# Kernel optimization log

Hardware: AMD Instinct MI355X
Metric: run time of the kernel (lower is better)

The kernel has to match this reference:

```python
import jax, jax.numpy as jnp
import numpy as np

B, N = 2, 8192
D_POINTS, D_MODEL, K = 64, 128, 16


def _lin(key, fi, fo):
    return jax.random.normal(key, (fi, fo), jnp.float32) / np.sqrt(fi)


def setup_inputs() -> dict:
    key = jax.random.key(0)
    ks = jax.random.split(key, 16)
    return {
        "xyz": jax.random.normal(ks[0], (B, N, 3), jnp.float32),
        "normals": jax.random.normal(ks[1], (B, N, 3), jnp.float32),
        "features": jax.random.normal(ks[2], (B, N, D_POINTS), jnp.float32),
        "fc1_w": _lin(ks[3], D_POINTS, D_MODEL), "fc1_b": jnp.zeros((D_MODEL,), jnp.float32),
        "fc2_w": _lin(ks[4], D_MODEL, D_POINTS), "fc2_b": jnp.zeros((D_POINTS,), jnp.float32),
        "gamma_w1": _lin(ks[5], D_MODEL, D_MODEL), "gamma_b1": jnp.zeros((D_MODEL,), jnp.float32),
        "gamma_w2": _lin(ks[6], D_MODEL, D_MODEL), "gamma_b2": jnp.zeros((D_MODEL,), jnp.float32),
        "delta_w1": _lin(ks[7], 3, D_MODEL), "delta_b1": jnp.zeros((D_MODEL,), jnp.float32),
        "delta_w2": _lin(ks[8], D_MODEL, D_MODEL), "delta_b2": jnp.zeros((D_MODEL,), jnp.float32),
        "wq": _lin(ks[9], D_MODEL, D_MODEL),
        "wk": _lin(ks[10], D_MODEL, D_MODEL),
        "wv": _lin(ks[11], D_MODEL, D_MODEL),
    }


def _gather(points, idx):
    # points: (b, n, c), idx: (b, n, k) -> (b, n, k, c)
    b, n, c = points.shape
    k = idx.shape[-1]
    flat = jnp.take_along_axis(points, idx.reshape(b, n * k, 1), axis=1)
    return flat.reshape(b, n, k, c)


def reference(xyz, normals, features, fc1_w, fc1_b, fc2_w, fc2_b,
              gamma_w1, gamma_b1, gamma_w2, gamma_b2,
              delta_w1, delta_b1, delta_w2, delta_b2, wq, wk, wv):
    # pairwise squared distances (b, n, n)
    sq = jnp.sum(xyz * xyz, axis=-1)
    dists = sq[:, :, None] + sq[:, None, :] - 2.0 * jnp.einsum('bnd,bmd->bnm', xyz, xyz)
    _, knn_idx = jax.lax.top_k(-dists, K)  # k smallest distances (includes self)

    knn_xyz = _gather(xyz, knn_idx)                      # (b, n, k, 3)
    x = features @ fc1_w + fc1_b                         # (b, n, d_model)
    q = x @ wq                                           # (b, n, d_model)
    k_nbr = _gather(x @ wk, knn_idx)                     # (b, n, k, d_model)
    v_nbr = _gather(x @ wv, knn_idx)                     # (b, n, k, d_model)

    # positional encoding: fc_delta(rel_pos), ends with ReLU
    rel = xyz[:, :, None, :] - knn_xyz                   # (b, n, k, 3)
    pos_enc = jax.nn.relu(jax.nn.relu(rel @ delta_w1 + delta_b1) @ delta_w2 + delta_b2)

    # vector attention logits: fc_gamma(q - k + pos_enc)
    h = q[:, :, None, :] - k_nbr + pos_enc
    logits = jax.nn.relu(h @ gamma_w1 + gamma_b1) @ gamma_w2 + gamma_b2
    attn = jax.nn.softmax(logits / np.sqrt(D_MODEL), axis=-2)  # softmax over neighbors

    res = jnp.einsum('bnkf,bnkf->bnf', attn, v_nbr + pos_enc)
    res = res @ fc2_w + fc2_b + features
    return res, attn
```

## Files before the change

### kernel.cpp

```cpp
#include <hip/hip_runtime.h>
#include <cstdint>

typedef unsigned long long ull;
typedef __bf16 bf16x8 __attribute__((ext_vector_type(8)));
typedef float f32x4 __attribute__((ext_vector_type(4)));
typedef float f32x2 __attribute__((ext_vector_type(2)));

#define NPTS 8192
#define NB 2
#define KNN 16
#define DM 128
#define PADK 136

__device__ __forceinline__ float sq3f(float x, float y, float z) {
    return __fadd_rn(__fadd_rn(__fmul_rn(x, x), __fmul_rn(y, y)), __fmul_rn(z, z));
}
__device__ __forceinline__ unsigned ford(unsigned u) {
    return (u & 0x80000000u) ? ~u : (u | 0x80000000u);
}
__device__ __forceinline__ float inv_ford(unsigned f) {
    unsigned u = (f & 0x80000000u) ? (f ^ 0x80000000u) : ~f;
    return __uint_as_float(u);
}
__device__ __forceinline__ f32x2 pk_mul(f32x2 a, f32x2 b) {
    f32x2 d;
    asm("v_pk_mul_f32 %0, %1, %2" : "=v"(d) : "v"(a), "v"(b));
    return d;
}
__device__ __forceinline__ f32x2 pk_add(f32x2 a, f32x2 b) {
    f32x2 d;
    asm("v_pk_add_f32 %0, %1, %2" : "=v"(d) : "v"(a), "v"(b));
    return d;
}

__global__ __launch_bounds__(256) void knn_kernel(const float* __restrict__ xyz,
                                                  int* __restrict__ idx_out) {
    __shared__ float4 xsA[512];
    __shared__ float4 xsB[512];
    const int t = threadIdx.x;
    const int wv = t >> 6, lane = t & 63;
    const int q_id = blockIdx.x * 4 + wv;
    const int b = q_id >> 13;
    const int i = q_id & (NPTS - 1);
    const float* xb = xyz + (size_t)b * NPTS * 3;
    const float qx = xb[3 * i + 0], qy = xb[3 * i + 1], qz = xb[3 * i + 2];
    const float sqi = sq3f(qx, qy, qz);
    const f32x2 qx2 = {qx, qx}, qy2 = {qy, qy}, qz2 = {qz, qz};
    const f32x2 sqi2 = {sqi, sqi}, ntwo2 = {-2.0f, -2.0f};

    unsigned list_hi = 0xffffffffu, list_lo = 0xffffffffu;
    float thrF = __uint_as_float(0x7f800000u);

#define INSERT(FC, CKLO)                                                                 \
    {                                                                                    \
        unsigned ck_hi = ford(__float_as_uint(FC));                                      \
        unsigned ck_lo = (CKLO);                                                         \
        unsigned ph = __shfl_up(list_hi, 1);                                             \
        unsigned pl = __shfl_up(list_lo, 1);                                             \
        bool lt = (ck_hi < list_hi) || (ck_hi == list_hi && ck_lo < list_lo);            \
        bool ge = (lane == 0) || (ck_hi > ph) || (ck_hi == ph && ck_lo >= pl);           \
        list_hi = lt ? (ge ? ck_hi : ph) : list_hi;                                      \
        list_lo = lt ? (ge ? ck_lo : pl) : list_lo;                                      \
        unsigned th = (unsigned)__builtin_amdgcn_readlane((int)list_hi, 15);             \
        th = (th > 0xff800000u) ? 0xff800000u : th;            \
        thrF = fminf(thrF, inv_ford(th));                                                \
    }

    for (int ch = 0; ch < 8; ++ch) {
        __syncthreads();
#pragma unroll
        for (int e = 0; e < 2; e++) {
            int s = t + e * 256;
            int c0 = ((s >> 6) << 7) + (s & 63);
            int g = ch * 1024 + c0;
            float x0 = xb[3 * g + 0], y0 = xb[3 * g + 1], z0 = xb[3 * g + 2];
            float x1 = xb[3 * (g + 64) + 0], y1 = xb[3 * (g + 64) + 1], z1 = xb[3 * (g + 64) + 2];
            xsA[s] = make_float4(x0, x1, y0, y1);
            xsB[s] = make_float4(z0, z1, sq3f(x0, y0, z0), sq3f(x1, y1, z1));
        }
        __syncthreads();
        for (int m = 0; m < 8; m++) {
            const int s = m * 64 + lane;
            float4 A = xsA[s];
            float4 B = xsB[s];
            f32x2 ax = {A.x, A.y}, ay = {A.z, A.w};
            f32x2 bz = {B.x, B.y}, bs = {B.z, B.w};
            f32x2 p1 = pk_mul(qx2, ax);
            f32x2 p2 = pk_mul(qy2, ay);
            f32x2 p3 = pk_mul(qz2, bz);
            f32x2 s1 = pk_add(p1, p2);
            f32x2 s2 = pk_add(s1, p3);
            f32x2 num = pk_add(sqi2, bs);
            f32x2 tm = pk_mul(ntwo2, s2);
            f32x2 dd = pk_add(num, tm);
            float dA = dd.x, dB = dd.y;
            if (ch == 0 && m == 0) {
                float mn = fminf(dA, dB);
                mn = fminf(mn, __shfl_xor(mn, 1));
                mn = fminf(mn, __shfl_xor(mn, 2));
                float mx = mn;
                mx = fmaxf(mx, __shfl_xor(mx, 4));
                mx = fmaxf(mx, __shfl_xor(mx, 8));
                mx = fmaxf(mx, __shfl_xor(mx, 16));
                mx = fmaxf(mx, __shfl_xor(mx, 32));
                thrF = mx;
            }
            ull balA = __ballot(dA <= thrF);
            ull balB = __ballot(dB <= thrF);
            if ((balA | balB) == 0ull) continue;
            const unsigned jbase = (unsigned)(ch * 1024 + m * 128);
            while (balA) {
                int l = (int)__builtin_ctzll(balA);
                balA &= balA - 1;
                float fc = __uint_as_float(
                    (unsigned)__builtin_amdgcn_readlane(__float_as_int(dA), l));
                if (fc <= thrF) INSERT(fc, jbase + (unsigned)l)
            }
            while (balB) {
                int l = (int)__builtin_ctzll(balB);
                balB &= balB - 1;
                float fc = __uint_as_float(
                    (unsigned)__builtin_amdgcn_readlane(__float_as_int(dB), l));
                if (fc <= thrF) INSERT(fc, jbase + 64u + (unsigned)l)
            }
        }
    }
#undef INSERT
    if (lane < 16)
        idx_out[q_id * 16 + lane] = (int)list_lo;
}

__global__ __launch_bounds__(256) void wprep_kernel(const float* __restrict__ d2,
                                                    const float* __restrict__ g1,
                                                    const float* __restrict__ g2,
                                                    const float* __restrict__ wq,
                                                    const float* __restrict__ wk,
                                                    const float* __restrict__ wv,
                                                    __bf16* __restrict__ d2t,
                                                    __bf16* __restrict__ g1t,
                                                    __bf16* __restrict__ g2t,
                                                    __bf16* __restrict__ wqt,
                                                    __bf16* __restrict__ wkt,
                                                    __bf16* __restrict__ wvt) {
    const int bi = blockIdx.x;
    const float* src = (bi == 0) ? d2 : (bi == 1) ? g1 : (bi == 2) ? g2
                     : (bi == 3) ? wq : (bi == 4) ? wk : wv;
    __bf16* dst = (bi == 0) ? d2t : (bi == 1) ? g1t : (bi == 2) ? g2t
                : (bi == 3) ? wqt : (bi == 4) ? wkt : wvt;
#pragma unroll
    for (int e = 0; e < 64; e++) {
        int id = threadIdx.x + e * 256;
        int k = id >> 7, n = id & 127;
        dst[n * 128 + k] = (__bf16)src[id];
    }
}

#define STAGE_W(SRC)                                                                       \
    {                                                                                      \
        _Pragma("unroll")                                                                  \
        for (int e = 0; e < 8; e++) {                                                      \
            int ch = t + e * 256;                                                          \
            int r = ch >> 4, ck = ch & 15;                                                 \
            *(bf16x8*)&Wb[r * PADK + ck * 8] = *(const bf16x8*)&SRC[r * 128 + ck * 8];     \
        }                                                                                  \
    }

__global__ __launch_bounds__(256, 1) void xqkv_kernel(const float* __restrict__ feats,
                                                      const float* __restrict__ fc1_w,
                                                      const float* __restrict__ fc1_b,
                                                      const __bf16* __restrict__ wqt,
                                                      const __bf16* __restrict__ wkt,
                                                      const __bf16* __restrict__ wvt,
                                                      float* __restrict__ qo,
                                                      float* __restrict__ ko,
                                                      float* __restrict__ vo) {
    __shared__ __align__(16) char lds[52224];
    float* At = (float*)lds;
    float* Wt = (float*)(lds + 16640);
    __bf16* Ab = (__bf16*)lds;
    __bf16* Wb = (__bf16*)(lds + 17408);
    const int t = threadIdx.x;
    const int base = blockIdx.x * 64;

#pragma unroll
    for (int e = 0; e < 16; e++) {
        int id = t + e * 256;
        int r = id >> 6, c = id & 63;
        At[c * 65 + r] = feats[(size_t)(base + r) * 64 + c];
    }
#pragma unroll
    for (int e = 0; e < 32; e++) { int id = t + e * 256; Wt[id] = fc1_w[id]; }
    __syncthreads();
    const int r0 = (t >> 4) * 4;
    const int c0 = (t & 15) * 8;
    float acc[4][8];
#pragma unroll
    for (int i = 0; i < 4; i++)
#pragma unroll
        for (int j = 0; j < 8; j++) acc[i][j] = fc1_b[c0 + j];
#pragma unroll 4
    for (int kk = 0; kk < 64; ++kk) {
        float a0 = At[kk * 65 + r0 + 0];
        float a1 = At[kk * 65 + r0 + 1];
        float a2 = At[kk * 65 + r0 + 2];
        float a3 = At[kk * 65 + r0 + 3];
        const float4 w0 = *(const float4*)&Wt[kk * 128 + c0];
        const float4 w1 = *(const float4*)&Wt[kk * 128 + c0 + 4];
        float wj[8] = {w0.x, w0.y, w0.z, w0.w, w1.x, w1.y, w1.z, w1.w};
#pragma unroll
        for (int j = 0; j < 8; j++) {
            acc[0][j] += a0 * wj[j];
            acc[1][j] += a1 * wj[j];
            acc[2][j] += a2 * wj[j];
            acc[3][j] += a3 * wj[j];
        }
    }
    __syncthreads();

#pragma unroll
    for (int i = 0; i < 4; i++)
#pragma unroll
        for (int j = 0; j < 8; j++)
            Ab[(r0 + i) * PADK + c0 + j] = (__bf16)acc[i][j];
    STAGE_W(wqt)
    __syncthreads();

    const int lane = t & 63;
    const int lr = lane & 15, lg = lane >> 4;
    const int rbase = (t >> 6) * 16;

#define QGEMM(ACC, OUT)                                                                    \
    {                                                                                      \
        f32x4 ACC[8];                                                                      \
        _Pragma("unroll")                                                                  \
        for (int ct = 0; ct < 8; ct++) ACC[ct] = (f32x4){0.f, 0.f, 0.f, 0.f};              \
        _Pragma("unroll")                                                                  \
        for (int kt = 0; kt < 4; kt++) {                                                   \
            const int ko = kt * 32 + 8 * lg;                                               \
            bf16x8 a0 = *(const bf16x8*)&Ab[(rbase + lr) * PADK + ko];                     \
            _Pragma("unroll")                                                              \
            for (int ct = 0; ct < 8; ct++) {                                               \
                bf16x8 bv = *(const bf16x8*)&Wb[(ct * 16 + lr) * PADK + ko];               \
                ACC[ct] = __builtin_amdgcn_mfma_f32_16x16x32_bf16(a0, bv, ACC[ct], 0, 0, 0); \
            }                                                                              \
        }                                                                                  \
        _Pragma("unroll")                                                                  \
        for (int ct = 0; ct < 8; ct++)                                                     \
            _Pragma("unroll")                                                              \
            for (int e = 0; e < 4; e++)                                                    \
                OUT[(size_t)(base + rbase + 4 * lg + e) * 128 + ct * 16 + lr] = ACC[ct][e]; \
    }

    QGEMM(accq, qo)
    __syncthreads();
    STAGE_W(wkt)
    __syncthreads();
    QGEMM(acck, ko)
    __syncthreads();
    STAGE_W(wvt)
    __syncthreads();
    QGEMM(accv, vo)
#undef QGEMM
}

#define DO_GEMM(ACC0, ACC1, WPTR)                                                          \
    {                                                                                      \
        _Pragma("unroll")                                                                  \
        for (int kt = 0; kt < 4; kt++) {                                                   \
            const int ko = kt * 32 + 8 * lg;                                               \
            bf16x8 a0 = *(const bf16x8*)&Ab[(rbase + lr) * PADK + ko];                     \
            bf16x8 a1 = *(const bf16x8*)&Ab[(rbase + 16 + lr) * PADK + ko];                \
            _Pragma("unroll")                                                              \
            for (int ct = 0; ct < 8; ct++) {                                               \
                bf16x8 bv = *(const bf16x8*)&WPTR[(ct * 16 + lr) * PADK + ko];             \
                ACC0[ct] = __builtin_amdgcn_mfma_f32_16x16x32_bf16(a0, bv, ACC0[ct], 0, 0, 0); \
                ACC1[ct] = __builtin_amdgcn_mfma_f32_16x16x32_bf16(a1, bv, ACC1[ct], 0, 0, 0); \
            }                                                                              \
        }                                                                                  \
    }

__global__ __launch_bounds__(256, 2) void k345_kernel(const float* __restrict__ xyz,
                                                      const int* __restrict__ idxw,
                                                      const float* __restrict__ q,
                                                      const float* __restrict__ xk,
                                                      const float* __restrict__ xv,
                                                      const float* __restrict__ d1,
                                                      const float* __restrict__ bd1,
                                                      const float* __restrict__ bd2,
                                                      const float* __restrict__ bg1,
                                                      const float* __restrict__ bg2,
                                                      const __bf16* __restrict__ d2t,
                                                      const __bf16* __restrict__ g1t,
                                                      const __bf16* __restrict__ g2t,
                                                      float* __restrict__ attn,
                                                      float* __restrict__ res_pre) {
    __shared__ __bf16 Ab[128 * PADK];
    __shared__ __bf16 Wb[128 * PADK];
    __shared__ float rels[128 * 4];
    __shared__ int jrow[128];
    __shared__ float d1s[3 * 128];
    __shared__ float bd1s[128], bd2s[128], bg1s[128], bg2s[128];

    const int t = threadIdx.x;
    const int wv = t >> 6;
    const int lane = t & 63;
    const int lr = lane & 15, lg = lane >> 4;
    const int R0 = blockIdx.x * 128;
    const int b = R0 >> 17;
    const int rbase = wv * 32;

#pragma unroll
    for (int e = 0; e < 2; e++) { int id = t + e * 256; if (id < 384) d1s[id] = d1[id]; }
    if (t < 128) {
        bd1s[t] = bd1[t]; bd2s[t] = bd2[t]; bg1s[t] = bg1[t]; bg2s[t] = bg2[t];
    } else {
        int r = t - 128;
        int j = idxw[R0 + r];
        jrow[r] = j;
        const float* pn = xyz + (size_t)((R0 + r) >> 4) * 3;
        const float* pj = xyz + (size_t)((b << 13) + j) * 3;
        rels[r * 4 + 0] = pn[0] - pj[0];
        rels[r * 4 + 1] = pn[1] - pj[1];
        rels[r * 4 + 2] = pn[2] - pj[2];
    }
    STAGE_W(d2t)
    __syncthreads();

    {
        const int c = t & 127;
        const float w0 = d1s[c], w1 = d1s[128 + c], w2 = d1s[256 + c], bb = bd1s[c];
#pragma unroll
        for (int e = 0; e < 64; e++) {
            int r = (t >> 7) + e * 2;
            float v = fmaf(rels[r * 4 + 2], w2,
                      fmaf(rels[r * 4 + 1], w1, fmaf(rels[r * 4 + 0], w0, bb)));
            Ab[r * PADK + c] = (__bf16)fmaxf(v, 0.0f);
        }
    }
    __syncthreads();

    f32x4 acc0[8], acc1[8];
#pragma unroll
    for (int ct = 0; ct < 8; ct++) {
        float bb = bd2s[ct * 16 + lr];
        acc0[ct] = (f32x4){bb, bb, bb, bb};
        acc1[ct] = acc0[ct];
    }
    DO_GEMM(acc0, acc1, Wb)
    f32x4 pos0[8], pos1[8];
#pragma unroll
    for (int ct = 0; ct < 8; ct++) {
#pragma unroll
        for (int e = 0; e < 4; e++) {
            pos0[ct][e] = fmaxf(acc0[ct][e], 0.0f);
            pos1[ct][e] = fmaxf(acc1[ct][e], 0.0f);
        }
    }

#pragma unroll
    for (int rt = 0; rt < 2; rt++) {
        const int rloc = rbase + rt * 16 + 4 * lg;
        const size_t qbase = (size_t)((R0 + rloc) >> 4) * 128;
        const int j0 = jrow[rloc + 0], j1 = jrow[rloc + 1];
        const int j2 = jrow[rloc + 2], j3 = jrow[rloc + 3];
        const size_t kb0 = (size_t)((b << 13) + j0) * 128;
        const size_t kb1 = (size_t)((b << 13) + j1) * 128;
        const size_t kb2 = (size_t)((b << 13) + j2) * 128;
        const size_t kb3 = (size_t)((b << 13) + j3) * 128;
        f32x4* posR = rt ? pos1 : pos0;
#pragma unroll
        for (int ct = 0; ct < 8; ct++) {
            const int c = ct * 16 + lr;
            const float qv = q[qbase + c];
            f32x4 p = posR[ct];
            Ab[(rloc + 0) * PADK + c] = (__bf16)(p[0] + qv - xk[kb0 + c]);
            Ab[(rloc + 1) * PADK + c] = (__bf16)(p[1] + qv - xk[kb1 + c]);
            Ab[(rloc + 2) * PADK + c] = (__bf16)(p[2] + qv - xk[kb2 + c]);
            Ab[(rloc + 3) * PADK + c] = (__bf16)(p[3] + qv - xk[kb3 + c]);
        }
    }
    __syncthreads();
    STAGE_W(g1t)
    __syncthreads();

#pragma unroll
    for (int ct = 0; ct < 8; ct++) {
        float bb = bg1s[ct * 16 + lr];
        acc0[ct] = (f32x4){bb, bb, bb, bb};
        acc1[ct] = acc0[ct];
    }
    DO_GEMM(acc0, acc1, Wb)
#pragma unroll
    for (int rt = 0; rt < 2; rt++) {
        const int rloc = rbase + rt * 16 + 4 * lg;
        f32x4* accR = rt ? acc1 : acc0;
#pragma unroll
        for (int ct = 0; ct < 8; ct++) {
            const int c = ct * 16 + lr;
            f32x4 p = accR[ct];
            Ab[(rloc + 0) * PADK + c] = (__bf16)fmaxf(p[0], 0.0f);
            Ab[(rloc + 1) * PADK + c] = (__bf16)fmaxf(p[1], 0.0f);
            Ab[(rloc + 2) * PADK + c] = (__bf16)fmaxf(p[2], 0.0f);
            Ab[(rloc + 3) * PADK + c] = (__bf16)fmaxf(p[3], 0.0f);
        }
    }
    __syncthreads();
    STAGE_W(g2t)
    __syncthreads();

#pragma unroll
    for (int ct = 0; ct < 8; ct++) {
        float bb = bg2s[ct * 16 + lr];
        acc0[ct] = (f32x4){bb, bb, bb, bb};
        acc1[ct] = acc0[ct];
    }
    DO_GEMM(acc0, acc1, Wb)
    const float scale = 0.08838834764831845f;
#pragma unroll
    for (int rt = 0; rt < 2; rt++) {
        const int rloc = rbase + rt * 16 + 4 * lg;
        const int j0 = jrow[rloc + 0], j1 = jrow[rloc + 1];
        const int j2 = jrow[rloc + 2], j3 = jrow[rloc + 3];
        const size_t vb0 = (size_t)((b << 13) + j0) * 128;
        const size_t vb1 = (size_t)((b << 13) + j1) * 128;
        const size_t vb2 = (size_t)((b << 13) + j2) * 128;
        const size_t vb3 = (size_t)((b << 13) + j3) * 128;
        f32x4* accR = rt ? acc1 : acc0;
        f32x4* posR = rt ? pos1 : pos0;
#pragma unroll
        for (int ct = 0; ct < 8; ct++) {
            const int c = ct * 16 + lr;
            f32x4 p = accR[ct];
            float l0 = p[0] * scale, l1 = p[1] * scale, l2 = p[2] * scale, l3 = p[3] * scale;
            float m = fmaxf(fmaxf(l0, l1), fmaxf(l2, l3));
            m = fmaxf(m, __shfl_xor(m, 16));
            m = fmaxf(m, __shfl_xor(m, 32));
            float e0 = __expf(l0 - m), e1 = __expf(l1 - m);
            float e2 = __expf(l2 - m), e3 = __expf(l3 - m);
            float s = (e0 + e1) + (e2 + e3);
            s += __shfl_xor(s, 16);
            s += __shfl_xor(s, 32);
            float inv = 1.0f / s;
            float a0 = e0 * inv, a1 = e1 * inv, a2 = e2 * inv, a3 = e3 * inv;
            size_t ob = (size_t)(R0 + rloc) * 128 + c;
            attn[ob + 0 * 128] = a0;
            attn[ob + 1 * 128] = a1;
            attn[ob + 2 * 128] = a2;
            attn[ob + 3 * 128] = a3;
            f32x4 pp = posR[ct];
            float r = a0 * (xv[vb0 + c] + pp[0])
                    + a1 * (xv[vb1 + c] + pp[1])
                    + a2 * (xv[vb2 + c] + pp[2])
                    + a3 * (xv[vb3 + c] + pp[3]);
            r += __shfl_xor(r, 16);
            r += __shfl_xor(r, 32);
            if (lg == 0)
                res_pre[(size_t)((R0 >> 4) + wv * 2 + rt) * 128 + c] = r;
        }
    }
}

__global__ __launch_bounds__(256, 1) void k6_kernel(const float* __restrict__ res_pre,
                                                    const float* __restrict__ w,
                                                    const float* __restrict__ bias,
                                                    const float* __restrict__ feats,
                                                    float* __restrict__ res_out) {
    __shared__ float At[128 * 65];
    __shared__ __align__(16) float Wt[128 * 64];
    const int t = threadIdx.x;
    const int base = blockIdx.x * 64;
#pragma unroll
    for (int e = 0; e < 32; e++) {
        int id = t + e * 256;
        int r = id >> 7, c = id & 127;
        At[c * 65 + r] = res_pre[(size_t)(base + r) * 128 + c];
    }
#pragma unroll
    for (int e = 0; e < 32; e++) { int id = t + e * 256; Wt[id] = w[id]; }
    __syncthreads();
    const int r0 = (t >> 4) * 4;
    const int c0 = (t & 15) * 4;
    float acc[4][4];
#pragma unroll
    for (int i = 0; i < 4; i++)
#pragma unroll
        for (int j = 0; j < 4; j++) acc[i][j] = bias[c0 + j];
#pragma unroll 4
    for (int kk = 0; kk < 128; ++kk) {
        float a0 = At[kk * 65 + r0 + 0];
        float a1 = At[kk * 65 + r0 + 1];
        float a2 = At[kk * 65 + r0 + 2];
        float a3 = At[kk * 65 + r0 + 3];
        const float4 w0 = *(const float4*)&Wt[kk * 64 + c0];
        float wj[4] = {w0.x, w0.y, w0.z, w0.w};
#pragma unroll
        for (int j = 0; j < 4; j++) {
            acc[0][j] += a0 * wj[j];
            acc[1][j] += a1 * wj[j];
            acc[2][j] += a2 * wj[j];
            acc[3][j] += a3 * wj[j];
        }
    }
#pragma unroll
    for (int i = 0; i < 4; i++)
#pragma unroll
        for (int j = 0; j < 4; j++)
            res_out[(size_t)(base + r0 + i) * 64 + c0 + j] =
                acc[i][j] + feats[(size_t)(base + r0 + i) * 64 + c0 + j];
}

extern "C" void kernel_launch(void* const* d_in, const int* in_sizes, int n_in,
                              void* d_out, int out_size, void* d_ws, size_t ws_size,
                              hipStream_t stream) {
    (void)in_sizes; (void)n_in; (void)out_size; (void)ws_size;
    const float* xyz   = (const float*)d_in[0];
    const float* feats = (const float*)d_in[2];
    const float* fc1_w = (const float*)d_in[3];
    const float* fc1_b = (const float*)d_in[4];
    const float* fc2_w = (const float*)d_in[5];
    const float* fc2_b = (const float*)d_in[6];
    const float* g1    = (const float*)d_in[7];
    const float* bg1   = (const float*)d_in[8];
    const float* g2    = (const float*)d_in[9];
    const float* bg2   = (const float*)d_in[10];
    const float* d1    = (const float*)d_in[11];
    const float* bd1   = (const float*)d_in[12];
    const float* d2    = (const float*)d_in[13];
    const float* bd2   = (const float*)d_in[14];
    const float* wq    = (const float*)d_in[15];
    const float* wk    = (const float*)d_in[16];
    const float* wv    = (const float*)d_in[17];

    int* idxw   = (int*)d_ws;
    float* qbuf = (float*)((char*)d_ws + (1 << 20));
    float* kbuf = qbuf + 2097152;
    float* vbuf = kbuf + 2097152;
    float* rpre = vbuf + 2097152;
    __bf16* d2t = (__bf16*)(rpre + 2097152);
    __bf16* g1t = d2t + 16384;
    __bf16* g2t = g1t + 16384;
    __bf16* wqt = g2t + 16384;
    __bf16* wkt = wqt + 16384;
    __bf16* wvt = wkt + 16384;

    float* res_out = (float*)d_out;
    float* attn    = res_out + 1048576;

    wprep_kernel<<<6, 256, 0, stream>>>(d2, g1, g2, wq, wk, wv,
                                        d2t, g1t, g2t, wqt, wkt, wvt);
    knn_kernel<<<4096, 256, 0, stream>>>(xyz, idxw);
    xqkv_kernel<<<256, 256, 0, stream>>>(feats, fc1_w, fc1_b, wqt, wkt, wvt,
                                         qbuf, kbuf, vbuf);
    k345_kernel<<<2048, 256, 0, stream>>>(xyz, idxw, qbuf, kbuf, vbuf, d1, bd1, bd2, bg1, bg2,
                                          d2t, g1t, g2t, attn, rpre);
    k6_kernel<<<256, 256, 0, stream>>>(rpre, fc2_w, fc2_b, feats, res_out);
}
```

Baseline: 244.5 us.

## Merge KNN and QKV projection into one launch with block-index dispatch

Combines the KNN search kernel and the x/q/k/v projection kernel into a single launch. The first 256 blocks run the projection and the rest run the KNN, so the small GEMM work overlaps the KNN instead of running after it. The projection no longer stages weights in LDS and reads fc1_w and the bf16 q/k/v weights straight from global memory. This shrinks shared memory to 17 KB and allows higher occupancy (launch bound 6). The trade-off is uncoalesced or repeated global weight reads, plus possible register pressure from the shared launch bound.

```diff
diff --git a/kernel.cpp b/kernel.cpp
--- a/kernel.cpp
+++ b/kernel.cpp
@@ -33,13 +33,14 @@
     return d;
 }
 
-__global__ __launch_bounds__(256) void knn_kernel(const float* __restrict__ xyz,
-                                                  int* __restrict__ idx_out) {
-    __shared__ float4 xsA[512];
-    __shared__ float4 xsB[512];
+__device__ __forceinline__ void knn_body(const float* __restrict__ xyz,
+                                         int* __restrict__ idx_out,
+                                         char* lds, int bid) {
+    float4* xsA = (float4*)lds;
+    float4* xsB = (float4*)(lds + 8192);
     const int t = threadIdx.x;
     const int wv = t >> 6, lane = t & 63;
-    const int q_id = blockIdx.x * 4 + wv;
+    const int q_id = bid * 4 + wv;
     const int b = q_id >> 13;
     const int i = q_id & (NPTS - 1);
     const float* xb = xyz + (size_t)b * NPTS * 3;
@@ -130,6 +131,111 @@
         idx_out[q_id * 16 + lane] = (int)list_lo;
 }
 
+__device__ __forceinline__ void xqkv_body(const float* __restrict__ feats,
+                                          const float* __restrict__ fc1_w,
+                                          const float* __restrict__ fc1_b,
+                                          const __bf16* __restrict__ wqt,
+                                          const __bf16* __restrict__ wkt,
+                                          const __bf16* __restrict__ wvt,
+                                          float* __restrict__ qo,
+                                          float* __restrict__ kko,
+                                          float* __restrict__ vvo,
+                                          char* lds, int bid) {
+    float* At = (float*)lds;
+    __bf16* Ab = (__bf16*)lds;
+    const int t = threadIdx.x;
+    const int base = bid * 64;
+
+#pragma unroll
+    for (int e = 0; e < 16; e++) {
+        int id = t + e * 256;
+        int r = id >> 6, c = id & 63;
+        At[c * 65 + r] = feats[(size_t)(base + r) * 64 + c];
+    }
+    __syncthreads();
+    const int r0 = (t >> 4) * 4;
+    const int c0 = (t & 15) * 8;
+    float acc[4][8];
+#pragma unroll
+    for (int i = 0; i < 4; i++)
+#pragma unroll
+        for (int j = 0; j < 8; j++) acc[i][j] = fc1_b[c0 + j];
+#pragma unroll 4
+    for (int kk = 0; kk < 64; ++kk) {
+        float a0 = At[kk * 65 + r0 + 0];
+        float a1 = At[kk * 65 + r0 + 1];
+        float a2 = At[kk * 65 + r0 + 2];
+        float a3 = At[kk * 65 + r0 + 3];
+        const float4 w0 = *(const float4*)&fc1_w[kk * 128 + c0];
+        const float4 w1 = *(const float4*)&fc1_w[kk * 128 + c0 + 4];
+        float wj[8] = {w0.x, w0.y, w0.z, w0.w, w1.x, w1.y, w1.z, w1.w};
+#pragma unroll
+        for (int j = 0; j < 8; j++) {
+            acc[0][j] += a0 * wj[j];
+            acc[1][j] += a1 * wj[j];
+            acc[2][j] += a2 * wj[j];
+            acc[3][j] += a3 * wj[j];
+        }
+    }
+    __syncthreads();
+
+#pragma unroll
+    for (int i = 0; i < 4; i++)
+#pragma unroll
+        for (int j = 0; j < 8; j++)
+            Ab[(r0 + i) * PADK + c0 + j] = (__bf16)acc[i][j];
+    __syncthreads();
+
+    const int lane = t & 63;
+    const int lr = lane & 15, lg = lane >> 4;
+    const int rbase = (t >> 6) * 16;
+
+#define QGEMM(WPTR, OUT)                                                                   \
+    {                                                                                      \
+        f32x4 accg[8];                                                                     \
+        _Pragma("unroll")                                                                  \
+        for (int ct = 0; ct < 8; ct++) accg[ct] = (f32x4){0.f, 0.f, 0.f, 0.f};             \
+        _Pragma("unroll")                                                                  \
+        for (int kt = 0; kt < 4; kt++) {                                                   \
+            const int ko = kt * 32 + 8 * lg;                                               \
+            bf16x8 a0 = *(const bf16x8*)&Ab[(rbase + lr) * PADK + ko];                     \
+            _Pragma("unroll")                                                              \
+            for (int ct = 0; ct < 8; ct++) {                                               \
+                bf16x8 bv = *(const bf16x8*)&WPTR[(ct * 16 + lr) * 128 + ko];              \
+                accg[ct] = __builtin_amdgcn_mfma_f32_16x16x32_bf16(a0, bv, accg[ct], 0, 0, 0); \
+            }                                                                              \
+        }                                                                                  \
+        _Pragma("unroll")                                                                  \
+        for (int ct = 0; ct < 8; ct++)                                                     \
+            _Pragma("unroll")                                                              \
+            for (int e = 0; e < 4; e++)                                                    \
+                OUT[(size_t)(base + rbase + 4 * lg + e) * 128 + ct * 16 + lr] = accg[ct][e]; \
+    }
+
+    QGEMM(wqt, qo)
+    QGEMM(wkt, kko)
+    QGEMM(wvt, vvo)
+#undef QGEMM
+}
+
+__global__ __launch_bounds__(256, 6) void mega_kernel(const float* __restrict__ xyz,
+                                                      int* __restrict__ idxw,
+                                                      const float* __restrict__ feats,
+                                                      const float* __restrict__ fc1_w,
+                                                      const float* __restrict__ fc1_b,
+                                                      const __bf16* __restrict__ wqt,
+                                                      const __bf16* __restrict__ wkt,
+                                                      const __bf16* __restrict__ wvt,
+                                                      float* __restrict__ qo,
+                                                      float* __restrict__ kko,
+                                                      float* __restrict__ vvo) {
+    __shared__ __align__(16) char lds[17408];
+    if (blockIdx.x < 256)
+        xqkv_body(feats, fc1_w, fc1_b, wqt, wkt, wvt, qo, kko, vvo, lds, blockIdx.x);
+    else
+        knn_body(xyz, idxw, lds, blockIdx.x - 256);
+}
+
 __global__ __launch_bounds__(256) void wprep_kernel(const float* __restrict__ d2,
                                                     const float* __restrict__ g1,
                                                     const float* __restrict__ g2,
@@ -164,104 +270,6 @@
             *(bf16x8*)&Wb[r * PADK + ck * 8] = *(const bf16x8*)&SRC[r * 128 + ck * 8];     \
         }                                                                                  \
     }
-
-__global__ __launch_bounds__(256, 1) void xqkv_kernel(const float* __restrict__ feats,
-                                                      const float* __restrict__ fc1_w,
-                                                      const float* __restrict__ fc1_b,
-                                                      const __bf16* __restrict__ wqt,
-                                                      const __bf16* __restrict__ wkt,
-                                                      const __bf16* __restrict__ wvt,
-                                                      float* __restrict__ qo,
-                                                      float* __restrict__ ko,
-                                                      float* __restrict__ vo) {
-    __shared__ __align__(16) char lds[52224];
-    float* At = (float*)lds;
-    float* Wt = (float*)(lds + 16640);
-    __bf16* Ab = (__bf16*)lds;
-    __bf16* Wb = (__bf16*)(lds + 17408);
-    const int t = threadIdx.x;
-    const int base = blockIdx.x * 64;
-
-#pragma unroll
-    for (int e = 0; e < 16; e++) {
-        int id = t + e * 256;
-        int r = id >> 6, c = id & 63;
-        At[c * 65 + r] = feats[(size_t)(base + r) * 64 + c];
-    }
-#pragma unroll
-    for (int e = 0; e < 32; e++) { int id = t + e * 256; Wt[id] = fc1_w[id]; }
-    __syncthreads();
-    const int r0 = (t >> 4) * 4;
-    const int c0 = (t & 15) * 8;
-    float acc[4][8];
-#pragma unroll
-    for (int i = 0; i < 4; i++)
-#pragma unroll
-        for (int j = 0; j < 8; j++) acc[i][j] = fc1_b[c0 + j];
-#pragma unroll 4
-    for (int kk = 0; kk < 64; ++kk) {
-        float a0 = At[kk * 65 + r0 + 0];
-        float a1 = At[kk * 65 + r0 + 1];
-        float a2 = At[kk * 65 + r0 + 2];
-        float a3 = At[kk * 65 + r0 + 3];
-        const float4 w0 = *(const float4*)&Wt[kk * 128 + c0];
-        const float4 w1 = *(const float4*)&Wt[kk * 128 + c0 + 4];
-        float wj[8] = {w0.x, w0.y, w0.z, w0.w, w1.x, w1.y, w1.z, w1.w};
-#pragma unroll
-        for (int j = 0; j < 8; j++) {
-            acc[0][j] += a0 * wj[j];
-            acc[1][j] += a1 * wj[j];
-            acc[2][j] += a2 * wj[j];
-            acc[3][j] += a3 * wj[j];
-        }
-    }
-    __syncthreads();
-
-#pragma unroll
-    for (int i = 0; i < 4; i++)
-#pragma unroll
-        for (int j = 0; j < 8; j++)
-            Ab[(r0 + i) * PADK + c0 + j] = (__bf16)acc[i][j];
-    STAGE_W(wqt)
-    __syncthreads();
-
-    const int lane = t & 63;
-    const int lr = lane & 15, lg = lane >> 4;
-    const int rbase = (t >> 6) * 16;
-
-#define QGEMM(ACC, OUT)                                                                    \
-    {                                                                                      \
-        f32x4 ACC[8];                                                                      \
-        _Pragma("unroll")                                                                  \
-        for (int ct = 0; ct < 8; ct++) ACC[ct] = (f32x4){0.f, 0.f, 0.f, 0.f};              \
-        _Pragma("unroll")                                                                  \
-        for (int kt = 0; kt < 4; kt++) {                                                   \
-            const int ko = kt * 32 + 8 * lg;                                               \
-            bf16x8 a0 = *(const bf16x8*)&Ab[(rbase + lr) * PADK + ko];                     \
-            _Pragma("unroll")                                                              \
-            for (int ct = 0; ct < 8; ct++) {                                               \
-                bf16x8 bv = *(const bf16x8*)&Wb[(ct * 16 + lr) * PADK + ko];               \
-                ACC[ct] = __builtin_amdgcn_mfma_f32_16x16x32_bf16(a0, bv, ACC[ct], 0, 0, 0); \
-            }                                                                              \
-        }                                                                                  \
-        _Pragma("unroll")                                                                  \
-        for (int ct = 0; ct < 8; ct++)                                                     \
-            _Pragma("unroll")                                                              \
-            for (int e = 0; e < 4; e++)                                                    \
-                OUT[(size_t)(base + rbase + 4 * lg + e) * 128 + ct * 16 + lr] = ACC[ct][e]; \
-    }
-
-    QGEMM(accq, qo)
-    __syncthreads();
-    STAGE_W(wkt)
-    __syncthreads();
-    QGEMM(acck, ko)
-    __syncthreads();
-    STAGE_W(wvt)
-    __syncthreads();
-    QGEMM(accv, vo)
-#undef QGEMM
-}
 
 #define DO_GEMM(ACC0, ACC1, WPTR)                                                          \
     {                                                                                      \
@@ -548,9 +556,8 @@
 
     wprep_kernel<<<6, 256, 0, stream>>>(d2, g1, g2, wq, wk, wv,
                                         d2t, g1t, g2t, wqt, wkt, wvt);
-    knn_kernel<<<4096, 256, 0, stream>>>(xyz, idxw);
-    xqkv_kernel<<<256, 256, 0, stream>>>(feats, fc1_w, fc1_b, wqt, wkt, wvt,
-                                         qbuf, kbuf, vbuf);
+    mega_kernel<<<4352, 256, 0, stream>>>(xyz, idxw, feats, fc1_w, fc1_b,
+                                          wqt, wkt, wvt, qbuf, kbuf, vbuf);
     k345_kernel<<<2048, 256, 0, stream>>>(xyz, idxw, qbuf, kbuf, vbuf, d1, bd1, bd2, bg1, bg2,
                                           d2t, g1t, g2t, attn, rpre);
     k6_kernel<<<256, 256, 0, stream>>>(rpre, fc2_w, fc2_b, feats, res_out);
```

Result: no change. 247.9 us (+1.4%).
